# Kernel tuning notes

Measured on AMD Instinct MI355X. Metric: run time of the kernel, lower is better.

Reference implementation:

```python
import jax, jax.numpy as jnp
import numpy as np

B, RES, STRIDE = 256, 14, 2
IN_DIM, OUT_DIM, KEY_DIM, HEADS, ATTN_RATIO = 384, 512, 16, 12, 2.0
VAL_DIM = int(ATTN_RATIO * KEY_DIM)            # 32
KEY_ATTN = KEY_DIM * HEADS                     # 192
VAL_ATTN = VAL_DIM * HEADS                     # 384
KV_DIM = KEY_ATTN + VAL_ATTN                   # 576
N = RES * RES                                  # 196
NQ = ((RES - 1) // STRIDE + 1) ** 2            # 49
SCALE = KEY_DIM ** -0.5
BN_EPS = 1e-5


def _bias_idxs():
    ki, kj = np.meshgrid(np.arange(RES), np.arange(RES), indexing='ij')
    k_pos = np.stack([ki.ravel(), kj.ravel()])                 # (2, N)
    qi, qj = np.meshgrid(np.arange(0, RES, STRIDE), np.arange(0, RES, STRIDE), indexing='ij')
    q_pos = np.stack([qi.ravel(), qj.ravel()])                 # (2, NQ)
    rel = np.abs(q_pos[:, :, None] - k_pos[:, None, :])        # (2, NQ, N)
    return jnp.asarray(rel[0] * RES + rel[1], dtype=jnp.int32) # (NQ, N)


def setup_inputs() -> dict:
    key = jax.random.key(0)
    ks = jax.random.split(key, 20)
    f = jax.random.normal
    u = lambda k, s: jax.random.uniform(k, s, jnp.float32, 0.5, 1.5)
    return {
        'x': f(ks[0], (B, N, IN_DIM), jnp.float32),
        'kv_w': f(ks[1], (KV_DIM, IN_DIM), jnp.float32) * 0.05,
        'kv_g': u(ks[2], (KV_DIM,)), 'kv_b': f(ks[3], (KV_DIM,)) * 0.1,
        'kv_m': f(ks[4], (KV_DIM,)) * 0.1, 'kv_v': u(ks[5], (KV_DIM,)),
        'q_w': f(ks[6], (KEY_ATTN, IN_DIM), jnp.float32) * 0.05,
        'q_g': u(ks[7], (KEY_ATTN,)), 'q_b': f(ks[8], (KEY_ATTN,)) * 0.1,
        'q_m': f(ks[9], (KEY_ATTN,)) * 0.1, 'q_v': u(ks[10], (KEY_ATTN,)),
        'pj_w': f(ks[11], (OUT_DIM, VAL_ATTN), jnp.float32) * 0.05,
        'pj_g': u(ks[12], (OUT_DIM,)), 'pj_b': f(ks[13], (OUT_DIM,)) * 0.1,
        'pj_m': f(ks[14], (OUT_DIM,)) * 0.1, 'pj_v': u(ks[15], (OUT_DIM,)),
        'biases': f(ks[16], (HEADS, N), jnp.float32) * 0.1,
        'bias_idxs': _bias_idxs(),
    }


def _bn(x, g, b, m, v):
    # BatchNorm (eval mode, running stats), affine
    return (x - m) * (g * jax.lax.rsqrt(v + BN_EPS)) + b


def reference(x, kv_w, kv_g, kv_b, kv_m, kv_v,
              q_w, q_g, q_b, q_m, q_v,
              pj_w, pj_g, pj_b, pj_m, pj_v,
              biases, bias_idxs):
    Bsz, Nn, C = x.shape
    # kv = LinearNorm(x): (B, N, KV_DIM)
    kv = _bn(jnp.einsum('bnc,dc->bnd', x, kv_w), kv_g, kv_b, kv_m, kv_v)
    kv = kv.reshape(Bsz, Nn, HEADS, KEY_DIM + VAL_DIM)
    k = kv[..., :KEY_DIM].transpose(0, 2, 3, 1)   # (B, H, KD, N)
    v = kv[..., KEY_DIM:].transpose(0, 2, 1, 3)   # (B, H, N, VD)
    # q path: strided spatial downsample then LinearNorm
    xq = x.reshape(Bsz, RES, RES, C)[:, ::STRIDE, ::STRIDE].reshape(Bsz, -1, C)  # (B, NQ, C)
    q = _bn(jnp.einsum('bnc,dc->bnd', xq, q_w), q_g, q_b, q_m, q_v)
    q = q.reshape(Bsz, NQ, HEADS, KEY_DIM).transpose(0, 2, 1, 3)  # (B, H, NQ, KD)
    # gathered relative-position bias: (H, NQ, N)
    attn_bias = biases[:, bias_idxs]
    attn = jnp.einsum('bhqd,bhdk->bhqk', q, k) * SCALE + attn_bias
    attn = jax.nn.softmax(attn, axis=-1)
    out = jnp.einsum('bhqk,bhkd->bhqd', attn, v)                  # (B, H, NQ, VD)
    out = out.transpose(0, 2, 1, 3).reshape(Bsz, NQ, VAL_ATTN)
    # proj: SiLU -> LinearNorm
    out = jax.nn.silu(out)
    out = _bn(jnp.einsum('bnc,dc->bnd', out, pj_w), pj_g, pj_b, pj_m, pj_v)
    return out
```

## Files before the change

kernel.cpp:

```cpp
#include <hip/hip_runtime.h>
#include <hip/hip_bf16.h>


typedef __bf16 bf16;
typedef float f32x4 __attribute__((ext_vector_type(4)));
typedef __bf16 bf16x8 __attribute__((ext_vector_type(8)));
typedef __bf16 bf16x4 __attribute__((ext_vector_type(4)));

#define KV2_BLK 18816
#define KV2_VOFF 6272
#define Q2_BLK 1568
#define LOG2E 1.4426950408889634f
#define QSCALE 0.36067376022224085f

__device__ __forceinline__ void gl2lds16(const bf16* g, bf16* l) {
  __builtin_amdgcn_global_load_lds(
      (const __attribute__((address_space(1))) void*)g,
      (__attribute__((address_space(3))) void*)l, 16, 0, 0);
}

__global__ void cast_kernel(const float* __restrict__ src, bf16* __restrict__ dst, long n) {
  long i = ((long)blockIdx.x * 256 + threadIdx.x) * 8;
  if (i + 8 <= n) {
    f32x4 lo = *(const f32x4*)(src + i), hi = *(const f32x4*)(src + i + 4);
    bf16x8 t;
    t[0]=(bf16)lo[0]; t[1]=(bf16)lo[1]; t[2]=(bf16)lo[2]; t[3]=(bf16)lo[3];
    t[4]=(bf16)hi[0]; t[5]=(bf16)hi[1]; t[6]=(bf16)hi[2]; t[7]=(bf16)hi[3];
    *(bf16x8*)(dst + i) = t;
  }
}

__global__ void wcast_kernel(const float* __restrict__ kv_w, const float* __restrict__ q_w,
                             const float* __restrict__ pj_w, bf16* __restrict__ kvwb,
                             bf16* __restrict__ qwb, bf16* __restrict__ pjwb) {
  long i = ((long)blockIdx.x * 256 + threadIdx.x) * 8;
  const float* s; bf16* d; long off;
  if (i < 221184)      { s = kv_w; d = kvwb; off = 0; }
  else if (i < 294912) { s = q_w;  d = qwb;  off = 221184; }
  else if (i < 491520) { s = pj_w; d = pjwb; off = 294912; }
  else return;
  long j = i - off;
  f32x4 lo = *(const f32x4*)(s + j), hi = *(const f32x4*)(s + j + 4);
  bf16x8 t;
  t[0]=(bf16)lo[0]; t[1]=(bf16)lo[1]; t[2]=(bf16)lo[2]; t[3]=(bf16)lo[3];
  t[4]=(bf16)hi[0]; t[5]=(bf16)hi[1]; t[6]=(bf16)hi[2]; t[7]=(bf16)hi[3];
  *(bf16x8*)(d + j) = t;
}

__global__ void prep_kernel(const float* kv_g, const float* kv_b, const float* kv_m, const float* kv_v,
                            const float* q_g,  const float* q_b,  const float* q_m,  const float* q_v,
                            const float* p_g,  const float* p_b,  const float* p_m,  const float* p_v,
                            float* scbuf) {
  int i = blockIdx.x * 256 + threadIdx.x;
  const float *g, *bb, *mm, *vv;
  float *sc, *sh;
  int c;
  float f = 1.0f;
  if (i < 576)        { c = i;       g = kv_g; bb = kv_b; mm = kv_m; vv = kv_v; sc = scbuf;        sh = scbuf + 576;  }
  else if (i < 768)   { c = i - 576; g = q_g;  bb = q_b;  mm = q_m;  vv = q_v;  sc = scbuf + 1152; sh = scbuf + 1344; f = QSCALE; }
  else if (i < 1280)  { c = i - 768; g = p_g;  bb = p_b;  mm = p_m;  vv = p_v;  sc = scbuf + 1536; sh = scbuf + 2048; }
  else return;
  float sv = g[c] * rsqrtf(vv[c] + 1e-5f);
  sc[c] = sv * f;
  sh[c] = (bb[c] - mm[c] * sv) * f;
}

__global__ void bias_kernel(const float* biases, const int* idxs, float* biasp2) {
  int i = blockIdx.x * 256 + threadIdx.x;
  if (i >= 39936) return;
  int lane = i & 63;
  int jt   = (i >> 6) % 13;
  int hw   = i / (13 * 64);
  int wid  = hw & 3;
  int h    = hw >> 2;
  int mrow = lane & 15, quad = lane >> 4;
  int c = jt * 16 + mrow;
  f32x4 v;
#pragma unroll
  for (int reg = 0; reg < 4; ++reg) {
    int r = wid * 16 + quad * 4 + reg;
    float val;
    if (c >= 196)      val = -1e30f;
    else if (r < 49)   val = biases[h * 196 + idxs[r * 196 + c]] * LOG2E;
    else               val = 0.0f;
    v[reg] = val;
  }
  ((f32x4*)biasp2)[i] = v;
}

template<int EPI, bool GATHER>
__global__ __launch_bounds__(128)
void gemm_bn_kernel(const bf16* __restrict__ A, const bf16* __restrict__ W,
                    const float* __restrict__ sc, const float* __restrict__ sh,
                    char* __restrict__ out, int N) {
  __shared__ __attribute__((aligned(16))) bf16 As[128 * 32];
  __shared__ __attribute__((aligned(16))) bf16 Ws[64 * 32];
  const int tid  = threadIdx.x;
  const int lane = tid & 63;
  const int wid  = tid >> 6;
  const int m0 = blockIdx.x * 128;
  const int n0 = blockIdx.y * 64;
  const int rquad = lane >> 2;
  const int kslot = lane & 3;

  long gA[4]; int lA[4];
#pragma unroll
  for (int i = 0; i < 4; ++i) {
    int rt = wid * 64 + i * 16 + rquad;
    long arow;
    if (GATHER) {
      int m = m0 + rt;
      int b = m / 49;
      int qq = m - b * 49;
      arow = (long)b * 196 + (qq / 7) * 28 + (qq % 7) * 2;
    } else {
      arow = m0 + rt;
    }
    gA[i] = arow * 384 + kslot * 8;
    lA[i] = (wid * 64 + i * 16) * 32;
  }
  long gW[2]; int lW[2];
#pragma unroll
  for (int j = 0; j < 2; ++j) {
    int rt = wid * 32 + j * 16 + rquad;
    gW[j] = (long)(n0 + rt) * 384 + kslot * 8;
    lW[j] = (wid * 32 + j * 16) * 32;
  }

  f32x4 acc[4][4] = {};
  const int mrow = lane & 15;
  const int quad = lane >> 4;

  for (int k0 = 0; k0 < 384; k0 += 32) {
#pragma unroll
    for (int i = 0; i < 4; ++i) gl2lds16(A + gA[i] + k0, As + lA[i]);
#pragma unroll
    for (int j = 0; j < 2; ++j) gl2lds16(W + gW[j] + k0, Ws + lW[j]);
    __syncthreads();

    bf16x8 af[4], bw[4];
#pragma unroll
    for (int mi = 0; mi < 4; ++mi)
      af[mi] = *(const bf16x8*)(As + (wid * 64 + mi * 16 + mrow) * 32 + quad * 8);
#pragma unroll
    for (int ni = 0; ni < 4; ++ni)
      bw[ni] = *(const bf16x8*)(Ws + (ni * 16 + mrow) * 32 + quad * 8);
#pragma unroll
    for (int mi = 0; mi < 4; ++mi)
#pragma unroll
      for (int ni = 0; ni < 4; ++ni)
        acc[mi][ni] = __builtin_amdgcn_mfma_f32_16x16x32_bf16(af[mi], bw[ni], acc[mi][ni], 0, 0, 0);
    __syncthreads();
  }

#pragma unroll
  for (int ni = 0; ni < 4; ++ni) {
    int col = n0 + ni * 16 + mrow;
    float s = sc[col], t = sh[col];
    int h = 0, dd = 0;
    if (EPI == 1) { h = col / 48; dd = col - h * 48; }
    if (EPI == 2) { h = col >> 4; dd = col & 15; }
#pragma unroll
    for (int mi = 0; mi < 4; ++mi) {
      int mbase = m0 + wid * 64 + mi * 16 + quad * 4;
      if (EPI == 0) {
#pragma unroll
        for (int reg = 0; reg < 4; ++reg) {
          int m = mbase + reg;
          ((float*)out)[(long)m * N + col] = acc[mi][ni][reg] * s + t;
        }
      } else if (EPI == 1) {
        int b = mbase / 196, j = mbase - b * 196;
        char* base = out + ((long)(b * 12 + h)) * KV2_BLK;
        if (dd < 16) {
#pragma unroll
          for (int reg = 0; reg < 4; ++reg)
            ((bf16*)base)[(j + reg) * 16 + dd] = (bf16)(acc[mi][ni][reg] * s + t);
        } else {
          bf16x4 tv;
#pragma unroll
          for (int reg = 0; reg < 4; ++reg)
            tv[reg] = (bf16)(acc[mi][ni][reg] * s + t);
          *(bf16x4*)((bf16*)(base + KV2_VOFF) + (dd - 16) * 196 + j) = tv;
        }
      } else {
#pragma unroll
        for (int reg = 0; reg < 4; ++reg) {
          int m = mbase + reg;
          int b = m / 49, qq = m - b * 49;
          ((bf16*)(out + ((long)(b * 12 + h)) * Q2_BLK))[qq * 16 + dd] = (bf16)(acc[mi][ni][reg] * s + t);
        }
      }
    }
  }
}

__global__ __launch_bounds__(256, 4)
void attn_kernel(const char* __restrict__ kv2, const char* __restrict__ qb2,
                 const float* __restrict__ biasp2, bf16* __restrict__ aout) {
  __shared__ __attribute__((aligned(16))) char smem[40448];
  bf16* vT_s = (bf16*)smem;
  bf16* k_s  = (bf16*)(smem + 12800);
  bf16* P_s  = (bf16*)(smem + 12800);

  const int bh = blockIdx.x;
  const int b = bh / 12;
  const int h = bh - b * 12;
  const int tid  = threadIdx.x;
  const int lane = tid & 63;
  const int wid  = tid >> 6;
  const int mrow = lane & 15;
  const int quad = lane >> 4;

  const bf16* ksrc = (const bf16*)(kv2 + (long)bh * KV2_BLK);
  const bf16* vsrc = (const bf16*)(kv2 + (long)bh * KV2_BLK + KV2_VOFF);
  const bf16* qsrc = (const bf16*)(qb2 + (long)bh * Q2_BLK);

  bf16x8 z = {};
  const int qrow = wid * 16 + mrow;
  bf16x8 aq = (quad < 2 && qrow < 49)
                  ? *(const bf16x8*)(qsrc + qrow * 16 + quad * 8) : z;
  f32x4 cb[13];
  {
    const f32x4* bf2 = (const f32x4*)biasp2 + ((long)(h * 4 + wid) * 13 * 64 + lane);
#pragma unroll
    for (int jt = 0; jt < 13; ++jt) cb[jt] = bf2[jt * 64];
  }

  {
    for (int i = tid; i < 832; i += 256) {
      int r = i >> 2, c = i & 3;
      *(bf16x8*)(k_s + r * 40 + c * 8) =
          (r < 196 && c < 2) ? *(const bf16x8*)(ksrc + r * 16 + c * 8) : z;
    }
    bf16x4 z4 = {};
    for (int i = tid; i < 1600; i += 256) {
      int r = i / 50, c = i - r * 50;
      *(bf16x4*)(vT_s + r * 200 + c * 4) =
          (c < 49) ? *(const bf16x4*)(vsrc + r * 196 + c * 4) : z4;
    }
  }
  __syncthreads();

  f32x4 s[13];
#pragma unroll
  for (int jt = 0; jt < 13; ++jt) {
    bf16x8 bk = *(const bf16x8*)(k_s + (jt * 16 + mrow) * 40 + quad * 8);
    s[jt] = __builtin_amdgcn_mfma_f32_16x16x32_bf16(aq, bk, cb[jt], 0, 0, 0);
  }

  const int rbase = wid * 16 + quad * 4;
  float mx[4], sm[4];
#pragma unroll
  for (int reg = 0; reg < 4; ++reg) {
    float m = -1e30f;
#pragma unroll
    for (int jt = 0; jt < 13; ++jt) m = fmaxf(m, s[jt][reg]);
    m = fmaxf(m, __shfl_xor(m, 1));
    m = fmaxf(m, __shfl_xor(m, 2));
    m = fmaxf(m, __shfl_xor(m, 4));
    m = fmaxf(m, __shfl_xor(m, 8));
    mx[reg] = m;
  }
#pragma unroll
  for (int jt = 0; jt < 13; ++jt)
#pragma unroll
    for (int reg = 0; reg < 4; ++reg)
      s[jt][reg] = __builtin_amdgcn_exp2f(s[jt][reg] - mx[reg]);
#pragma unroll
  for (int reg = 0; reg < 4; ++reg) {
    float t = 0.0f;
#pragma unroll
    for (int jt = 0; jt < 13; ++jt) t += s[jt][reg];
    t += __shfl_xor(t, 1);
    t += __shfl_xor(t, 2);
    t += __shfl_xor(t, 4);
    t += __shfl_xor(t, 8);
    sm[reg] = 1.0f / t;
  }

  __syncthreads();

  bf16* Pw = P_s + wid * 16 * 216;
#pragma unroll
  for (int jt = 0; jt < 13; ++jt) {
#pragma unroll
    for (int reg = 0; reg < 4; ++reg)
      Pw[(quad * 4 + reg) * 216 + jt * 16 + mrow] = (bf16)s[jt][reg];
  }

  f32x4 o[2] = {};
#pragma unroll
  for (int kk = 0; kk < 6; ++kk) {
    bf16x8 ap = *(const bf16x8*)(Pw + mrow * 216 + kk * 32 + quad * 8);
#pragma unroll
    for (int nt = 0; nt < 2; ++nt) {
      bf16x8 bv = *(const bf16x8*)(vT_s + (nt * 16 + mrow) * 200 + kk * 32 + quad * 8);
      o[nt] = __builtin_amdgcn_mfma_f32_16x16x32_bf16(ap, bv, o[nt], 0, 0, 0);
    }
  }
  {
    bf16x8 ap = (quad == 0) ? *(const bf16x8*)(Pw + mrow * 216 + 192) : z;
#pragma unroll
    for (int nt = 0; nt < 2; ++nt) {
      bf16x8 bv = (quad == 0) ? *(const bf16x8*)(vT_s + (nt * 16 + mrow) * 200 + 192) : z;
      o[nt] = __builtin_amdgcn_mfma_f32_16x16x32_bf16(ap, bv, o[nt], 0, 0, 0);
    }
  }

#pragma unroll
  for (int nt = 0; nt < 2; ++nt) {
#pragma unroll
    for (int reg = 0; reg < 4; ++reg) {
      int r = rbase + reg;
      if (r < 49) {
        float x = o[nt][reg] * sm[reg];
        float sil = x / (1.0f + __expf(-x));
        aout[((long)b * 49 + r) * 384 + h * 32 + nt * 16 + mrow] = (bf16)sil;
      }
    }
  }
}

extern "C" void kernel_launch(void* const* d_in, const int* in_sizes, int n_in,
                              void* d_out, int out_size, void* d_ws, size_t ws_size,
                              hipStream_t stream) {
  const float* x      = (const float*)d_in[0];
  const float* kv_w   = (const float*)d_in[1];
  const float* q_w    = (const float*)d_in[6];
  const float* pj_w   = (const float*)d_in[11];
  const float* biases = (const float*)d_in[16];
  const int*   bidx   = (const int*)d_in[17];

  char* ws = (char*)d_ws;
  float* scbuf = (float*)ws;
  char*  qb2   = ws + 471296;
  bf16*  aout  = (bf16*)(ws + 5288192);
  bf16*  xb    = (bf16*)(ws + 14921984);
  bf16*  kvwb  = (bf16*)(ws + 53457152);
  bf16*  qwb   = (bf16*)(ws + 53899520);
  bf16*  pjwb  = (bf16*)(ws + 54046976);
  char*  kv2   = ws + 54440192;
  float* biasp2= (float*)(ws + 112242944);

  cast_kernel<<<9408, 256, 0, stream>>>(x, xb, 19267584L);
  wcast_kernel<<<240, 256, 0, stream>>>(kv_w, q_w, pj_w, kvwb, qwb, pjwb);

  prep_kernel<<<5, 256, 0, stream>>>(
      (const float*)d_in[2],  (const float*)d_in[3],  (const float*)d_in[4],  (const float*)d_in[5],
      (const float*)d_in[7],  (const float*)d_in[8],  (const float*)d_in[9],  (const float*)d_in[10],
      (const float*)d_in[12], (const float*)d_in[13], (const float*)d_in[14], (const float*)d_in[15],
      scbuf);
  bias_kernel<<<156, 256, 0, stream>>>(biases, bidx, biasp2);

  gemm_bn_kernel<2, true><<<dim3(98, 3), 128, 0, stream>>>(
      xb, qwb, scbuf + 1152, scbuf + 1344, qb2, 192);

  gemm_bn_kernel<1, false><<<dim3(392, 9), 128, 0, stream>>>(
      xb, kvwb, scbuf, scbuf + 576, kv2, 576);

  attn_kernel<<<3072, 256, 0, stream>>>(kv2, qb2, biasp2, aout);

  gemm_bn_kernel<0, false><<<dim3(98, 8), 128, 0, stream>>>(
      aout, pjwb, scbuf + 1536, scbuf + 2048, (char*)d_out, 512);
}
```

Measured before the change: 277.4 us.

## Double-buffer GEMM A tiles in LDS and load W fragments directly into registers

The GEMM kernel now uses 256-thread blocks covering 256 rows, double-buffers the A tile in LDS so the next k-slice loads while MFMAs run on the current one, and drops the W LDS tile in favour of per-lane register loads straight from global memory, prefetched one step ahead. This targets the load-then-compute stall of the old single-buffered loop and removes one of its two barriers per k-step. In exchange it uses more LDS and registers per block and launches half as many blocks. Each wave also re-reads W from global/L2 on its own.

```diff
diff --git a/kernel.cpp b/kernel.cpp
--- a/kernel.cpp
+++ b/kernel.cpp
@@ -89,19 +89,20 @@
 }
 
 template<int EPI, bool GATHER>
-__global__ __launch_bounds__(128)
+__global__ __launch_bounds__(256)
 void gemm_bn_kernel(const bf16* __restrict__ A, const bf16* __restrict__ W,
                     const float* __restrict__ sc, const float* __restrict__ sh,
                     char* __restrict__ out, int N) {
-  __shared__ __attribute__((aligned(16))) bf16 As[128 * 32];
-  __shared__ __attribute__((aligned(16))) bf16 Ws[64 * 32];
+  __shared__ __attribute__((aligned(16))) bf16 As[2 * 256 * 32];
   const int tid  = threadIdx.x;
   const int lane = tid & 63;
   const int wid  = tid >> 6;
-  const int m0 = blockIdx.x * 128;
+  const int m0 = blockIdx.x * 256;
   const int n0 = blockIdx.y * 64;
   const int rquad = lane >> 2;
   const int kslot = lane & 3;
+  const int mrow = lane & 15;
+  const int quad = lane >> 4;
 
   long gA[4]; int lA[4];
 #pragma unroll
@@ -119,38 +120,39 @@
     gA[i] = arow * 384 + kslot * 8;
     lA[i] = (wid * 64 + i * 16) * 32;
   }
-  long gW[2]; int lW[2];
-#pragma unroll
-  for (int j = 0; j < 2; ++j) {
-    int rt = wid * 32 + j * 16 + rquad;
-    gW[j] = (long)(n0 + rt) * 384 + kslot * 8;
-    lW[j] = (wid * 32 + j * 16) * 32;
-  }
+  const bf16* Wp = W + (long)(n0 + mrow) * 384 + quad * 8;
 
   f32x4 acc[4][4] = {};
-  const int mrow = lane & 15;
-  const int quad = lane >> 4;
-
-  for (int k0 = 0; k0 < 384; k0 += 32) {
-#pragma unroll
-    for (int i = 0; i < 4; ++i) gl2lds16(A + gA[i] + k0, As + lA[i]);
-#pragma unroll
-    for (int j = 0; j < 2; ++j) gl2lds16(W + gW[j] + k0, Ws + lW[j]);
+
+#pragma unroll
+  for (int i = 0; i < 4; ++i) gl2lds16(A + gA[i], As + lA[i]);
+  bf16x8 bwc[4], bwn[4];
+#pragma unroll
+  for (int ni = 0; ni < 4; ++ni) bwc[ni] = *(const bf16x8*)(Wp + ni * 6144);
+  __syncthreads();
+
+#pragma unroll
+  for (int t = 0; t < 12; ++t) {
+    const int ca = (t & 1) * 8192;
+    if (t < 11) {
+      const long kg = (long)(t + 1) * 32;
+#pragma unroll
+      for (int i = 0; i < 4; ++i) gl2lds16(A + gA[i] + kg, As + (8192 - ca) + lA[i]);
+#pragma unroll
+      for (int ni = 0; ni < 4; ++ni) bwn[ni] = *(const bf16x8*)(Wp + ni * 6144 + kg);
+    }
+    bf16x8 af[4];
+#pragma unroll
+    for (int mi = 0; mi < 4; ++mi)
+      af[mi] = *(const bf16x8*)(As + ca + (wid * 64 + mi * 16 + mrow) * 32 + quad * 8);
+#pragma unroll
+    for (int mi = 0; mi < 4; ++mi)
+#pragma unroll
+      for (int ni = 0; ni < 4; ++ni)
+        acc[mi][ni] = __builtin_amdgcn_mfma_f32_16x16x32_bf16(af[mi], bwc[ni], acc[mi][ni], 0, 0, 0);
     __syncthreads();
-
-    bf16x8 af[4], bw[4];
-#pragma unroll
-    for (int mi = 0; mi < 4; ++mi)
-      af[mi] = *(const bf16x8*)(As + (wid * 64 + mi * 16 + mrow) * 32 + quad * 8);
-#pragma unroll
-    for (int ni = 0; ni < 4; ++ni)
-      bw[ni] = *(const bf16x8*)(Ws + (ni * 16 + mrow) * 32 + quad * 8);
-#pragma unroll
-    for (int mi = 0; mi < 4; ++mi)
-#pragma unroll
-      for (int ni = 0; ni < 4; ++ni)
-        acc[mi][ni] = __builtin_amdgcn_mfma_f32_16x16x32_bf16(af[mi], bw[ni], acc[mi][ni], 0, 0, 0);
-    __syncthreads();
+#pragma unroll
+    for (int ni = 0; ni < 4; ++ni) bwc[ni] = bwn[ni];
   }
 
 #pragma unroll
@@ -353,14 +355,14 @@
       scbuf);
   bias_kernel<<<156, 256, 0, stream>>>(biases, bidx, biasp2);
 
-  gemm_bn_kernel<2, true><<<dim3(98, 3), 128, 0, stream>>>(
+  gemm_bn_kernel<2, true><<<dim3(49, 3), 256, 0, stream>>>(
       xb, qwb, scbuf + 1152, scbuf + 1344, qb2, 192);
 
-  gemm_bn_kernel<1, false><<<dim3(392, 9), 128, 0, stream>>>(
+  gemm_bn_kernel<1, false><<<dim3(196, 9), 256, 0, stream>>>(
       xb, kvwb, scbuf, scbuf + 576, kv2, 576);
 
   attn_kernel<<<3072, 256, 0, stream>>>(kv2, qb2, biasp2, aout);
 
-  gemm_bn_kernel<0, false><<<dim3(98, 8), 128, 0, stream>>>(
+  gemm_bn_kernel<0, false><<<dim3(49, 8), 256, 0, stream>>>(
       aout, pjwb, scbuf + 1536, scbuf + 2048, (char*)d_out, 512);
 }
```

Result: slower. 305.8 us (+10.2%).

## Triple-buffer LDS tiles in GEMM with async prefetch two steps ahead

Applied to the files above, without the earlier changes.

Replaces the single-buffered load/sync/compute K-loop in the BN GEMM kernel with a three-stage LDS ring. Global-to-LDS loads run two K-steps ahead, and per-wave vmcnt waits replace the two __syncthreads per iteration with one s_barrier. Each wave now loads the whole W tile itself, so W traffic is duplicated, but no wave has to wait for another wave's loads. LDS use triples, which may reduce occupancy, and the hand-written waitcnt counts must match the number of loads issued per stage.

```diff
diff --git a/kernel.cpp b/kernel.cpp
--- a/kernel.cpp
+++ b/kernel.cpp
@@ -93,8 +93,8 @@
 void gemm_bn_kernel(const bf16* __restrict__ A, const bf16* __restrict__ W,
                     const float* __restrict__ sc, const float* __restrict__ sh,
                     char* __restrict__ out, int N) {
-  __shared__ __attribute__((aligned(16))) bf16 As[128 * 32];
-  __shared__ __attribute__((aligned(16))) bf16 Ws[64 * 32];
+  __shared__ __attribute__((aligned(16))) bf16 As[3 * 128 * 32];
+  __shared__ __attribute__((aligned(16))) bf16 Ws[3 * 64 * 32];
   const int tid  = threadIdx.x;
   const int lane = tid & 63;
   const int wid  = tid >> 6;
@@ -102,6 +102,8 @@
   const int n0 = blockIdx.y * 64;
   const int rquad = lane >> 2;
   const int kslot = lane & 3;
+  const int mrow = lane & 15;
+  const int quad = lane >> 4;
 
   long gA[4]; int lA[4];
 #pragma unroll
@@ -119,39 +121,53 @@
     gA[i] = arow * 384 + kslot * 8;
     lA[i] = (wid * 64 + i * 16) * 32;
   }
-  long gW[2]; int lW[2];
-#pragma unroll
-  for (int j = 0; j < 2; ++j) {
-    int rt = wid * 32 + j * 16 + rquad;
+  long gW[4]; int lW[4];
+#pragma unroll
+  for (int j = 0; j < 4; ++j) {
+    int rt = j * 16 + rquad;
     gW[j] = (long)(n0 + rt) * 384 + kslot * 8;
-    lW[j] = (wid * 32 + j * 16) * 32;
+    lW[j] = (j * 16) * 32;
   }
 
   f32x4 acc[4][4] = {};
-  const int mrow = lane & 15;
-  const int quad = lane >> 4;
-
-  for (int k0 = 0; k0 < 384; k0 += 32) {
-#pragma unroll
-    for (int i = 0; i < 4; ++i) gl2lds16(A + gA[i] + k0, As + lA[i]);
-#pragma unroll
-    for (int j = 0; j < 2; ++j) gl2lds16(W + gW[j] + k0, Ws + lW[j]);
-    __syncthreads();
-
+
+#define STAGE_T(buf, t)                                                     \
+  do {                                                                      \
+    const long kg_ = (long)(t) * 32;                                        \
+    _Pragma("unroll")                                                       \
+    for (int i_ = 0; i_ < 4; ++i_)                                          \
+      gl2lds16(A + gA[i_] + kg_, As + (buf) * 4096 + lA[i_]);               \
+    _Pragma("unroll")                                                       \
+    for (int j_ = 0; j_ < 4; ++j_)                                          \
+      gl2lds16(W + gW[j_] + kg_, Ws + (buf) * 2048 + lW[j_]);               \
+  } while (0)
+
+  STAGE_T(0, 0);
+  STAGE_T(1, 1);
+
+#pragma unroll
+  for (int t = 0; t < 12; ++t) {
+    asm volatile("s_barrier" ::: "memory");
+    if (t + 2 < 12) STAGE_T((t + 2) % 3, t + 2);
+    if (t < 10)       asm volatile("s_waitcnt vmcnt(16)" ::: "memory");
+    else if (t == 10) asm volatile("s_waitcnt vmcnt(8)"  ::: "memory");
+    else              asm volatile("s_waitcnt vmcnt(0)"  ::: "memory");
+    const int ca = (t % 3) * 4096;
+    const int cw = (t % 3) * 2048;
     bf16x8 af[4], bw[4];
 #pragma unroll
     for (int mi = 0; mi < 4; ++mi)
-      af[mi] = *(const bf16x8*)(As + (wid * 64 + mi * 16 + mrow) * 32 + quad * 8);
+      af[mi] = *(const bf16x8*)(As + ca + (wid * 64 + mi * 16 + mrow) * 32 + quad * 8);
 #pragma unroll
     for (int ni = 0; ni < 4; ++ni)
-      bw[ni] = *(const bf16x8*)(Ws + (ni * 16 + mrow) * 32 + quad * 8);
+      bw[ni] = *(const bf16x8*)(Ws + cw + (ni * 16 + mrow) * 32 + quad * 8);
 #pragma unroll
     for (int mi = 0; mi < 4; ++mi)
 #pragma unroll
       for (int ni = 0; ni < 4; ++ni)
         acc[mi][ni] = __builtin_amdgcn_mfma_f32_16x16x32_bf16(af[mi], bw[ni], acc[mi][ni], 0, 0, 0);
-    __syncthreads();
-  }
+  }
+#undef STAGE_T
 
 #pragma unroll
   for (int ni = 0; ni < 4; ++ni) {
```

After: 277.5 us. Within noise of the previous version (+0.1%).
